# Kernel optimization log

Hardware: AMD Instinct MI355X
Metric: run time of the kernel (lower is better)

The kernel has to match this reference:

```python
import jax, jax.numpy as jnp
import numpy as np

NUM_EMB = 1000
HIDDEN = 256
SCALE = 2
N_HEADS = 8
HEAD_DIM = HIDDEN * SCALE // N_HEADS  # 64
HS = HIDDEN * SCALE  # 512
EPS = 1e-6


def setup_inputs() -> dict:
    key = jax.random.key(0)
    ks = jax.random.split(key, 12)
    B, N, C, H, W = 8, 8, HIDDEN, 32, 32
    std = 0.02
    return {
        "q": jax.random.randint(ks[0], (B,), 0, NUM_EMB, dtype=jnp.int32),
        "c": jax.random.normal(ks[1], (B, N, C, H, W), dtype=jnp.float32),
        "rms_w": jnp.ones((HIDDEN,), dtype=jnp.float32),
        "emb": jax.random.normal(ks[2], (NUM_EMB, HIDDEN), dtype=jnp.float32) * std,
        "w1": jax.random.normal(ks[3], (HIDDEN, HS), dtype=jnp.float32) * std,
        "b1": jnp.zeros((HS,), dtype=jnp.float32),
        "w2": jax.random.normal(ks[4], (HS, HS), dtype=jnp.float32) * std,
        "b2": jnp.zeros((HS,), dtype=jnp.float32),
        "w_kv": jax.random.normal(ks[5], (HIDDEN, HS * 2), dtype=jnp.float32) * std,
        "w_out": jax.random.normal(ks[6], (HS, HIDDEN), dtype=jnp.float32) * std,
        "b_out": jnp.zeros((HIDDEN,), dtype=jnp.float32),
    }


def reference(q, c, rms_w, emb, w1, b1, w2, b2, w_kv, w_out, b_out):
    B, N, C, H, W = c.shape
    attn_scale = HEAD_DIM ** (-0.5)
    # permute to [B,H,W,N,C] and RMSNorm over channel dim
    c = jnp.transpose(c, (0, 3, 4, 1, 2))
    c = c * jax.lax.rsqrt(jnp.mean(c * c, axis=-1, keepdims=True) + EPS) * rms_w
    # query path: embed + gated MLP -> [B, n_heads, head_dim]
    qe = emb[q]                                   # [B, hidden]
    qh = jax.nn.silu(qe @ w1 + b1) @ w2 + b2      # [B, HS]
    qh = qh.reshape(B, N_HEADS, HEAD_DIM)
    # kv projection: [B,H,W,N, 2*HS] -> [B,H,W,n_heads,N, 2*head_dim]
    kv = (c @ w_kv).reshape(B, H, W, N, N_HEADS, 2 * HEAD_DIM)
    kv = jnp.transpose(kv, (0, 1, 2, 4, 3, 5))
    k, v = jnp.split(kv, 2, axis=-1)              # each [B,H,W,heads,N,head_dim]
    # broadcast per-pixel cross-attention: query shared over H,W
    dots = jnp.einsum('bed,bhwend->bhwen', qh, k) * attn_scale
    attn = jax.nn.softmax(dots, axis=-1)
    h = jnp.einsum('bhwen,bhwend->bhwed', attn, v)  # [B,H,W,heads,head_dim]
    h = h.reshape(B, H, W, HS)
    out = h @ w_out + b_out                        # [B,H,W,hidden]
    return jnp.transpose(out, (0, 3, 1, 2))        # [B,hidden,H,W]
```

## Files before the change

kernel.cpp:

```cpp
#include <hip/hip_runtime.h>

typedef _Float16 f16;
typedef _Float16 f16x4 __attribute__((ext_vector_type(4)));
typedef _Float16 f16x8 __attribute__((ext_vector_type(8)));
typedef float f32x4 __attribute__((ext_vector_type(4)));

static __device__ inline char* a_addr(char* Abase, int px, int k) {
    return Abase + px * 4096 + ((((k >> 3) ^ px) << 4) | ((k & 7) << 1));
}

__launch_bounds__(256)
__global__ void k_setup(const int* __restrict__ q, const float* __restrict__ emb,
                        const float* __restrict__ w1, const float* __restrict__ b1,
                        const float* __restrict__ w2, const float* __restrict__ b2,
                        const float* __restrict__ w_kv, const float* __restrict__ w_out,
                        const float* __restrict__ rms_w,
                        f16* __restrict__ qkw, f16* __restrict__ mtp) {
    int blk = blockIdx.x;
    int t = threadIdx.x;
    __shared__ float qe[256];
    __shared__ float x1L[512];
    __shared__ float ps[4][64];
    __shared__ float qhL[64];
    __shared__ float wv[64][8];

    if (blk < 64) {
        int b = blk >> 3, e = blk & 7;
        qe[t] = emb[(size_t)q[b] * 256 + t];
        __syncthreads();
        float a0 = b1[t], a1 = b1[t + 256];
        for (int c = 0; c < 256; ++c) {
            float qv = qe[c];
            a0 += qv * w1[c * 512 + t];
            a1 += qv * w1[c * 512 + t + 256];
        }
        x1L[t]       = a0 / (1.f + __expf(-a0));
        x1L[t + 256] = a1 / (1.f + __expf(-a1));
        __syncthreads();
        int d = t & 63, ks = t >> 6;
        float acc = 0.f;
        for (int k = ks * 128; k < ks * 128 + 128; ++k)
            acc += x1L[k] * w2[k * 512 + e * 64 + d];
        ps[ks][d] = acc;
        __syncthreads();
        if (t < 64)
            qhL[t] = b2[e * 64 + t] + ps[0][t] + ps[1][t] + ps[2][t] + ps[3][t];
        __syncthreads();
        const float* row = w_kv + (size_t)t * 1024 + e * 128;
        float a2 = 0.f;
#pragma unroll
        for (int dd = 0; dd < 64; dd += 4) {
            float4 wv4 = *(const float4*)(row + dd);
            a2 += qhL[dd] * wv4.x + qhL[dd + 1] * wv4.y + qhL[dd + 2] * wv4.z + qhL[dd + 3] * wv4.w;
        }
        qkw[(b * 8 + e) * 256 + t] = (f16)(a2 * rms_w[t]);
    } else {
        int mb = blk - 64;
        int e = mb >> 5, c0 = (mb & 31) * 8;
        {
            int d = t & 63, cc = t >> 6;
            wv[d][cc]     = w_kv[(size_t)(c0 + cc) * 1024 + e * 128 + 64 + d];
            wv[d][cc + 4] = w_kv[(size_t)(c0 + cc + 4) * 1024 + e * 128 + 64 + d];
        }
        __syncthreads();
        int o = t;
        float acc[8];
#pragma unroll
        for (int c = 0; c < 8; ++c) acc[c] = 0.f;
        for (int d = 0; d < 64; ++d) {
            float wo = w_out[(size_t)(e * 64 + d) * 256 + o];
            float4 wa = *(const float4*)&wv[d][0];
            float4 wb = *(const float4*)&wv[d][4];
            acc[0] += wa.x * wo; acc[1] += wa.y * wo; acc[2] += wa.z * wo; acc[3] += wa.w * wo;
            acc[4] += wb.x * wo; acc[5] += wb.y * wo; acc[6] += wb.z * wo; acc[7] += wb.w * wo;
        }
        f16x8 ov;
#pragma unroll
        for (int c = 0; c < 8; ++c) ov[c] = (f16)(acc[c] * rms_w[c0 + c]);
        *(f16x8*)(mtp + ((size_t)((e * 256 + c0) >> 3) * 256 + o) * 8) = ov;
    }
}

__launch_bounds__(512, 4)
__global__ void k_attn(const float* __restrict__ cin, const f16* __restrict__ qkw,
                       const f16* __restrict__ mtp, const float* __restrict__ b_out,
                       float* __restrict__ out) {
    int blk = blockIdx.x;
    int b = blk & 7;
    int hw0 = (blk >> 3) * 16;
    int t = threadIdx.x;
    int lane = t & 63, w = t >> 6;
    int m16 = lane & 15, quad = lane >> 4;

    __shared__ char A[16 * 4096];
    __shared__ float dotsP[8][8][16];
    __shared__ float wred[8][8][16];
    __shared__ float rinvL[16][8];

    int px = t & 15, cb = t >> 4;
    const float* cbase = cin + ((size_t)b * 8 * 256) * 1024 + hw0 + px;
    for (int g = 0; g < 8; ++g) {
        const float* src = cbase + ((size_t)(g * 256 + cb * 8) << 10);
        float v[8];
#pragma unroll
        for (int j = 0; j < 8; ++j) v[j] = src[(size_t)j << 10];
        float s = 0.f;
        f16x8 hv;
#pragma unroll
        for (int j = 0; j < 8; ++j) { s += v[j] * v[j]; hv[j] = (f16)v[j]; }
        *(f16x8*)a_addr(A, px, g * 256 + cb * 8) = hv;
        s += __shfl_xor(s, 16);
        s += __shfl_xor(s, 32);
        if (lane < 16) wred[w][g][px] = s;
    }
    __syncthreads();

    if (t < 128) {
        int p = t >> 3, n = t & 7;
        float ss = 0.f;
#pragma unroll
        for (int ww = 0; ww < 8; ++ww) ss += wred[ww][n][p];
        rinvL[p][n] = rsqrtf(ss * (1.f / 256.f) + 1e-6f);
    }
    {
        f32x4 d0 = {0.f, 0.f, 0.f, 0.f};
        const f16* qrow = qkw + (size_t)b * 2048 + (m16 & 7) * 256;
#pragma unroll
        for (int ks = 0; ks < 8; ++ks) {
            f16x8 a0  = *(const f16x8*)a_addr(A, m16, w * 256 + ks * 32 + quad * 8);
            f16x8 bfr = *(const f16x8*)(qrow + ks * 32 + quad * 8);
            d0 = __builtin_amdgcn_mfma_f32_16x16x32_f16(a0, bfr, d0, 0, 0, 0);
        }
        if (m16 < 8) {
#pragma unroll
            for (int r = 0; r < 4; ++r) dotsP[w][m16][quad * 4 + r] = d0[r];
        }
    }
    __syncthreads();

    if (t < 128) {
        int p = t >> 3, e = t & 7;
        float l[8];
#pragma unroll
        for (int n = 0; n < 8; ++n) l[n] = dotsP[n][e][p] * rinvL[p][n] * 0.125f;
        float mx = l[0];
#pragma unroll
        for (int n = 1; n < 8; ++n) mx = fmaxf(mx, l[n]);
        float s = 0.f;
#pragma unroll
        for (int n = 0; n < 8; ++n) { l[n] = __expf(l[n] - mx); s += l[n]; }
        float inv = 1.f / s;
#pragma unroll
        for (int n = 0; n < 8; ++n) dotsP[n][e][p] = l[n] * inv * rinvL[p][n];
    }
    __syncthreads();

    {
        int bpx = t & 15, c0 = (t >> 4) * 8;
        float at[8][8];
#pragma unroll
        for (int e = 0; e < 8; ++e)
#pragma unroll
            for (int n = 0; n < 8; ++n) at[e][n] = dotsP[n][e][bpx];
#pragma unroll
        for (int cc = 0; cc < 8; cc += 4) {
            int c = c0 + cc;
            float cv[8][4];
#pragma unroll
            for (int n = 0; n < 8; ++n) {
                f16x4 hv = *(const f16x4*)a_addr(A, bpx, n * 256 + c);
                cv[n][0] = (float)hv[0]; cv[n][1] = (float)hv[1];
                cv[n][2] = (float)hv[2]; cv[n][3] = (float)hv[3];
            }
#pragma unroll
            for (int e = 0; e < 8; ++e) {
                float r0 = 0.f, r1 = 0.f, r2 = 0.f, r3 = 0.f;
#pragma unroll
                for (int n = 0; n < 8; ++n) {
                    float an = at[e][n];
                    r0 += an * cv[n][0]; r1 += an * cv[n][1];
                    r2 += an * cv[n][2]; r3 += an * cv[n][3];
                }
                f16x4 ov; ov[0] = (f16)r0; ov[1] = (f16)r1; ov[2] = (f16)r2; ov[3] = (f16)r3;
                *(f16x4*)a_addr(A, bpx, e * 256 + c) = ov;
            }
        }
    }
    __syncthreads();

    {
        f32x4 acc[2];
        acc[0] = (f32x4){0.f, 0.f, 0.f, 0.f};
        acc[1] = (f32x4){0.f, 0.f, 0.f, 0.f};
#pragma unroll 8
        for (int ks = 0; ks < 64; ++ks) {
            int k = (ks >> 3) * 256 + (ks & 7) * 32 + quad * 8;
            f16x8 af = *(const f16x8*)a_addr(A, m16, k);
            int kchunk = k >> 3;
#pragma unroll
            for (int ot = 0; ot < 2; ++ot) {
                f16x8 bfr = *(const f16x8*)(mtp + ((size_t)kchunk * 256
                                            + w * 32 + ot * 16 + m16) * 8);
                acc[ot] = __builtin_amdgcn_mfma_f32_16x16x32_f16(af, bfr, acc[ot], 0, 0, 0);
            }
        }
#pragma unroll
        for (int ot = 0; ot < 2; ++ot) {
            int o = w * 32 + ot * 16 + m16;
            float bo = b_out[o];
            float4 vv = {acc[ot][0] + bo, acc[ot][1] + bo, acc[ot][2] + bo, acc[ot][3] + bo};
            *(float4*)(out + ((size_t)b * 256 + o) * 1024 + hw0 + quad * 4) = vv;
        }
    }
}

extern "C" void kernel_launch(void* const* d_in, const int* in_sizes, int n_in,
                              void* d_out, int out_size, void* d_ws, size_t ws_size,
                              hipStream_t stream) {
    (void)in_sizes; (void)n_in; (void)out_size; (void)ws_size;
    const int*   q     = (const int*)d_in[0];
    const float* c     = (const float*)d_in[1];
    const float* rms_w = (const float*)d_in[2];
    const float* emb   = (const float*)d_in[3];
    const float* w1    = (const float*)d_in[4];
    const float* b1    = (const float*)d_in[5];
    const float* w2    = (const float*)d_in[6];
    const float* b2    = (const float*)d_in[7];
    const float* w_kv  = (const float*)d_in[8];
    const float* w_out = (const float*)d_in[9];
    const float* b_out = (const float*)d_in[10];
    float* out = (float*)d_out;

    char* ws = (char*)d_ws;
    f16* qkw = (f16*)ws;
    f16* mtp = (f16*)(ws + 32768);

    k_setup<<<320, 256, 0, stream>>>(q, emb, w1, b1, w2, b2, w_kv, w_out, rms_w, qkw, mtp);
    k_attn <<<512, 512, 0, stream>>>(c, qkw, mtp, b_out, out);
}
```

Measured before the change: 187.4 us.

## Fuse RMS and softmax into the mix stage, prefetch B fragments, unroll loads

```diff
diff --git a/kernel.cpp b/kernel.cpp
--- a/kernel.cpp
+++ b/kernel.cpp
@@ -29,6 +29,7 @@
         qe[t] = emb[(size_t)q[b] * 256 + t];
         __syncthreads();
         float a0 = b1[t], a1 = b1[t + 256];
+#pragma unroll 4
         for (int c = 0; c < 256; ++c) {
             float qv = qe[c];
             a0 += qv * w1[c * 512 + t];
@@ -39,6 +40,7 @@
         __syncthreads();
         int d = t & 63, ks = t >> 6;
         float acc = 0.f;
+#pragma unroll 4
         for (int k = ks * 128; k < ks * 128 + 128; ++k)
             acc += x1L[k] * w2[k * 512 + e * 64 + d];
         ps[ks][d] = acc;
@@ -67,6 +69,7 @@
         float acc[8];
 #pragma unroll
         for (int c = 0; c < 8; ++c) acc[c] = 0.f;
+#pragma unroll 4
         for (int d = 0; d < 64; ++d) {
             float wo = w_out[(size_t)(e * 64 + d) * 256 + o];
             float4 wa = *(const float4*)&wv[d][0];
@@ -95,33 +98,35 @@
     __shared__ char A[16 * 4096];
     __shared__ float dotsP[8][8][16];
     __shared__ float wred[8][8][16];
-    __shared__ float rinvL[16][8];
 
     int px = t & 15, cb = t >> 4;
     const float* cbase = cin + ((size_t)b * 8 * 256) * 1024 + hw0 + px;
-    for (int g = 0; g < 8; ++g) {
-        const float* src = cbase + ((size_t)(g * 256 + cb * 8) << 10);
-        float v[8];
-#pragma unroll
-        for (int j = 0; j < 8; ++j) v[j] = src[(size_t)j << 10];
-        float s = 0.f;
-        f16x8 hv;
-#pragma unroll
-        for (int j = 0; j < 8; ++j) { s += v[j] * v[j]; hv[j] = (f16)v[j]; }
-        *(f16x8*)a_addr(A, px, g * 256 + cb * 8) = hv;
-        s += __shfl_xor(s, 16);
-        s += __shfl_xor(s, 32);
-        if (lane < 16) wred[w][g][px] = s;
+#pragma unroll
+    for (int g = 0; g < 8; g += 2) {
+        const float* s0 = cbase + ((size_t)(g * 256 + cb * 8) << 10);
+        const float* s1 = cbase + ((size_t)((g + 1) * 256 + cb * 8) << 10);
+        float v0[8], v1[8];
+#pragma unroll
+        for (int j = 0; j < 8; ++j) v0[j] = s0[(size_t)j << 10];
+#pragma unroll
+        for (int j = 0; j < 8; ++j) v1[j] = s1[(size_t)j << 10];
+        float sa = 0.f, sb = 0.f;
+        f16x8 h0, h1;
+#pragma unroll
+        for (int j = 0; j < 8; ++j) { sa += v0[j] * v0[j]; h0[j] = (f16)v0[j]; }
+#pragma unroll
+        for (int j = 0; j < 8; ++j) { sb += v1[j] * v1[j]; h1[j] = (f16)v1[j]; }
+        *(f16x8*)a_addr(A, px, g * 256 + cb * 8)       = h0;
+        *(f16x8*)a_addr(A, px, (g + 1) * 256 + cb * 8) = h1;
+        sa += __shfl_xor(sa, 16); sa += __shfl_xor(sa, 32);
+        sb += __shfl_xor(sb, 16); sb += __shfl_xor(sb, 32);
+        if (lane < 16) {
+            wred[w][g][px]     = sa;
+            wred[w][g + 1][px] = sb;
+        }
     }
     __syncthreads();
 
-    if (t < 128) {
-        int p = t >> 3, n = t & 7;
-        float ss = 0.f;
-#pragma unroll
-        for (int ww = 0; ww < 8; ++ww) ss += wred[ww][n][p];
-        rinvL[p][n] = rsqrtf(ss * (1.f / 256.f) + 1e-6f);
-    }
     {
         f32x4 d0 = {0.f, 0.f, 0.f, 0.f};
         const f16* qrow = qkw + (size_t)b * 2048 + (m16 & 7) * 256;
@@ -138,52 +143,50 @@
     }
     __syncthreads();
 
-    if (t < 128) {
-        int p = t >> 3, e = t & 7;
-        float l[8];
-#pragma unroll
-        for (int n = 0; n < 8; ++n) l[n] = dotsP[n][e][p] * rinvL[p][n] * 0.125f;
-        float mx = l[0];
-#pragma unroll
-        for (int n = 1; n < 8; ++n) mx = fmaxf(mx, l[n]);
-        float s = 0.f;
-#pragma unroll
-        for (int n = 0; n < 8; ++n) { l[n] = __expf(l[n] - mx); s += l[n]; }
-        float inv = 1.f / s;
-#pragma unroll
-        for (int n = 0; n < 8; ++n) dotsP[n][e][p] = l[n] * inv * rinvL[p][n];
-    }
-    __syncthreads();
+    f16x8 pb[4][2];
+#pragma unroll
+    for (int ks = 0; ks < 4; ++ks) {
+        int kchunk = ks * 4 + quad;
+#pragma unroll
+        for (int ot = 0; ot < 2; ++ot)
+            pb[ks][ot] = *(const f16x8*)(mtp + ((size_t)kchunk * 256
+                                         + w * 32 + ot * 16 + m16) * 8);
+    }
 
     {
         int bpx = t & 15, c0 = (t >> 4) * 8;
-        float at[8][8];
-#pragma unroll
-        for (int e = 0; e < 8; ++e)
-#pragma unroll
-            for (int n = 0; n < 8; ++n) at[e][n] = dotsP[n][e][bpx];
-#pragma unroll
-        for (int cc = 0; cc < 8; cc += 4) {
-            int c = c0 + cc;
-            float cv[8][4];
+        float rinv[8];
+#pragma unroll
+        for (int n = 0; n < 8; ++n) {
+            float ss = 0.f;
+#pragma unroll
+            for (int ww = 0; ww < 8; ++ww) ss += wred[ww][n][bpx];
+            rinv[n] = rsqrtf(ss * (1.f / 256.f) + 1e-6f);
+        }
+        f16x8 cv[8];
+#pragma unroll
+        for (int n = 0; n < 8; ++n)
+            cv[n] = *(const f16x8*)a_addr(A, bpx, n * 256 + c0);
+#pragma unroll
+        for (int e = 0; e < 8; ++e) {
+            float l[8];
+#pragma unroll
+            for (int n = 0; n < 8; ++n) l[n] = dotsP[n][e][bpx] * rinv[n] * 0.125f;
+            float mx = l[0];
+#pragma unroll
+            for (int n = 1; n < 8; ++n) mx = fmaxf(mx, l[n]);
+            float s = 0.f;
+#pragma unroll
+            for (int n = 0; n < 8; ++n) { l[n] = __expf(l[n] - mx); s += l[n]; }
+            float inv = 1.f / s;
+            f16x8 r = {};
 #pragma unroll
             for (int n = 0; n < 8; ++n) {
-                f16x4 hv = *(const f16x4*)a_addr(A, bpx, n * 256 + c);
-                cv[n][0] = (float)hv[0]; cv[n][1] = (float)hv[1];
-                cv[n][2] = (float)hv[2]; cv[n][3] = (float)hv[3];
+                f16 an = (f16)(l[n] * inv * rinv[n]);
+#pragma unroll
+                for (int j = 0; j < 8; ++j) r[j] += cv[n][j] * an;
             }
-#pragma unroll
-            for (int e = 0; e < 8; ++e) {
-                float r0 = 0.f, r1 = 0.f, r2 = 0.f, r3 = 0.f;
-#pragma unroll
-                for (int n = 0; n < 8; ++n) {
-                    float an = at[e][n];
-                    r0 += an * cv[n][0]; r1 += an * cv[n][1];
-                    r2 += an * cv[n][2]; r3 += an * cv[n][3];
-                }
-                f16x4 ov; ov[0] = (f16)r0; ov[1] = (f16)r1; ov[2] = (f16)r2; ov[3] = (f16)r3;
-                *(f16x4*)a_addr(A, bpx, e * 256 + c) = ov;
-            }
+            *(f16x8*)a_addr(A, bpx, e * 256 + c0) = r;
         }
     }
     __syncthreads();
@@ -192,8 +195,14 @@
         f32x4 acc[2];
         acc[0] = (f32x4){0.f, 0.f, 0.f, 0.f};
         acc[1] = (f32x4){0.f, 0.f, 0.f, 0.f};
+#pragma unroll
+        for (int ks = 0; ks < 4; ++ks) {
+            f16x8 af = *(const f16x8*)a_addr(A, m16, ks * 32 + quad * 8);
+            acc[0] = __builtin_amdgcn_mfma_f32_16x16x32_f16(af, pb[ks][0], acc[0], 0, 0, 0);
+            acc[1] = __builtin_amdgcn_mfma_f32_16x16x32_f16(af, pb[ks][1], acc[1], 0, 0, 0);
+        }
 #pragma unroll 8
-        for (int ks = 0; ks < 64; ++ks) {
+        for (int ks = 4; ks < 64; ++ks) {
             int k = (ks >> 3) * 256 + (ks & 7) * 32 + quad * 8;
             f16x8 af = *(const f16x8*)a_addr(A, m16, k);
             int kchunk = k >> 3;
```

Result: faster. 173.3 us (-7.5%).
